# Performance work log

Hardware: AMD Instinct MI355X
Metric: run time of the kernel (lower is better)

The kernel has to match this reference:

```python
import jax, jax.numpy as jnp
import numpy as np

N_NODES = 1_000_000
N_EDGES = 32_000_000


def setup_inputs() -> dict:
    key = jax.random.key(0)
    k1, k2, k3, k4, k5 = jax.random.split(key, 5)
    state = jax.random.normal(k1, (N_NODES, 1), dtype=jnp.float32)
    edge_src = jax.random.randint(k2, (N_EDGES,), 0, N_NODES, dtype=jnp.int64)
    edge_dst = jax.random.randint(k3, (N_EDGES,), 0, N_NODES, dtype=jnp.int64)
    W = jax.random.normal(k4, (1, 2), dtype=jnp.float32)
    b = jax.random.normal(k5, (1,), dtype=jnp.float32)
    return {"state": state, "edge_src": edge_src, "edge_dst": edge_dst, "W": W, "b": b}


def reference(state, edge_src, edge_dst, W, b):
    # neighbor_sum[dst] += state[src]  (irregular gather + scatter-add)
    n = state.shape[0]
    messages = state[edge_src, 0]                              # [E]
    neighbor_sum = jax.ops.segment_sum(messages, edge_dst, num_segments=n)  # [n]
    x = jnp.concatenate([state, neighbor_sum[:, None]], axis=1)  # [n, 2]
    return x @ W.T + b                                           # [n, 1]
```

## Files before the change

kernel.cpp:

```cpp
#include <hip/hip_runtime.h>
#include <hip/hip_fp16.h>


#define NB_SHIFT 14
#define RANGE    (1 << NB_SHIFT)
#define NBALL    64
#define TPB      512
#define IPT      8
#define TILE     (TPB * IPT)
#define NWAVES   (TPB / 64)
#define NREP     4
#define GSPL     2
#define BPB      (NREP * GSPL)

typedef int   iv4 __attribute__((ext_vector_type(4)));
typedef float fv4 __attribute__((ext_vector_type(4)));
typedef unsigned uv4 __attribute__((ext_vector_type(4)));
typedef unsigned uv2 __attribute__((ext_vector_type(2)));

__device__ __forceinline__ void lds_fadd(float* p, float v) {
    unsigned addr = (unsigned)(uintptr_t)p;
    asm volatile("ds_add_f32 %0, %1" :: "v"(addr), "v"(v) : "memory");
}

__device__ __forceinline__ void lds_drain() {
    asm volatile("s_waitcnt lgkmcnt(0)" ::: "memory");
    __builtin_amdgcn_sched_barrier(0);
}

__global__ void k_init_cursors(int* __restrict__ cursors) {
    cursors[threadIdx.x] = 0;
}

__global__ __launch_bounds__(256) void k_cvt(const float* __restrict__ state,
                                             unsigned short* __restrict__ sh, int n4) {
    int i = blockIdx.x * blockDim.x + threadIdx.x;
    if (i >= n4) return;
    fv4 v = *(const fv4*)(state + i * 4);
    ushort4 h;
    h.x = __half_as_ushort(__float2half_rn(v[0]));
    h.y = __half_as_ushort(__float2half_rn(v[1]));
    h.z = __half_as_ushort(__float2half_rn(v[2]));
    h.w = __half_as_ushort(__float2half_rn(v[3]));
    *(ushort4*)(sh + i * 4) = h;
}

__global__ __launch_bounds__(TPB) void k_partition(
    const unsigned short* __restrict__ sh,
    const int* __restrict__ src,
    const int* __restrict__ dst,
    unsigned* __restrict__ records,
    int* __restrict__ cursors,
    int n_edges, int capR)
{
    __shared__ unsigned stage[TILE];
    __shared__ int cnt[NBALL];
    __shared__ int sbase[NBALL];
    __shared__ int gbase[NBALL];

    const int tid = threadIdx.x;
    const int rep = blockIdx.x & (NREP - 1);
    if (tid < NBALL) cnt[tid] = 0;

    const long long e0 = (long long)blockIdx.x * TILE + (long long)tid * IPT;

    unsigned rec[IPT];
    int bk[IPT];
    int pos[IPT];

    if (e0 + IPT <= (long long)n_edges) {
        const long long i4 = e0 >> 2;
        iv4 sA = __builtin_nontemporal_load((const iv4*)src + i4);
        iv4 sB = __builtin_nontemporal_load((const iv4*)src + i4 + 1);
        iv4 dA = __builtin_nontemporal_load((const iv4*)dst + i4);
        iv4 dB = __builtin_nontemporal_load((const iv4*)dst + i4 + 1);
        int s[IPT] = { sA[0], sA[1], sA[2], sA[3], sB[0], sB[1], sB[2], sB[3] };
        int d[IPT] = { dA[0], dA[1], dA[2], dA[3], dB[0], dB[1], dB[2], dB[3] };
        unsigned v[IPT];
        #pragma unroll
        for (int k = 0; k < IPT; ++k) v[k] = sh[s[k]];
        #pragma unroll
        for (int k = 0; k < IPT; ++k) {
            bk[k]  = d[k] >> NB_SHIFT;
            rec[k] = (v[k] << NB_SHIFT) | (unsigned)(d[k] & (RANGE - 1));
        }
    } else {
        #pragma unroll
        for (int k = 0; k < IPT; ++k) {
            long long e = e0 + k;
            if (e < n_edges) {
                int d = dst[e];
                unsigned v = sh[src[e]];
                bk[k]  = d >> NB_SHIFT;
                rec[k] = (v << NB_SHIFT) | (unsigned)(d & (RANGE - 1));
            } else {
                bk[k] = -1; rec[k] = 0;
            }
        }
    }
    __syncthreads();

    #pragma unroll
    for (int k = 0; k < IPT; ++k)
        if (bk[k] >= 0) pos[k] = atomicAdd(&cnt[bk[k]], 1);
    __syncthreads();

    if (tid < NBALL) {
        int h = cnt[tid];
        int v = h;
        #pragma unroll
        for (int off = 1; off < 64; off <<= 1) {
            int u = __shfl_up(v, off);
            if (tid >= off) v += u;
        }
        sbase[tid] = v - h;
        int he = (h + 1) & ~1;
        gbase[tid] = atomicAdd(&cursors[(tid << 2) | rep], he);
    }
    __syncthreads();

    #pragma unroll
    for (int k = 0; k < IPT; ++k)
        if (bk[k] >= 0) stage[sbase[bk[k]] + pos[k]] = rec[k];
    __syncthreads();

    const int wid = tid >> 6, lane = tid & 63;
    for (int b = wid; b < NBALL; b += NWAVES) {
        const int sb = sbase[b], h = cnt[b], gb = gbase[b];
        const int hp = (h + 1) >> 1;
        unsigned* dstp = records + (size_t)((b << 2) | rep) * capR + gb;
        for (int j = lane; j < hp; j += 64) {
            uv2 r;
            r[0] = stage[sb + 2 * j];
            r[1] = (2 * j + 1 < h) ? stage[sb + 2 * j + 1] : 0u;
            *(uv2*)(dstp + 2 * j) = r;
        }
    }
}

__global__ __launch_bounds__(1024) void k_bins(
    const unsigned* __restrict__ records,
    const int* __restrict__ cursors,
    float* __restrict__ partial,
    int capR)
{
    __shared__ float bins[RANGE];
    const int b   = blockIdx.x / BPB;
    const int sub = blockIdx.x % BPB;
    const int rep = sub >> 1;
    const int g   = sub & 1;
    const int cnt = cursors[(b << 2) | rep];
    const size_t base = (size_t)((b << 2) | rep) * capR;
    const int lo = (int)((long long)cnt * g       / GSPL) & ~1;
    const int hi = (g == GSPL - 1) ? cnt : ((int)((long long)cnt * (g + 1) / GSPL) & ~1);
    const int tid = threadIdx.x;

    fv4* bins4 = (fv4*)bins;
    for (int i = tid; i < RANGE / 4; i += 1024) bins4[i] = (fv4){0.f, 0.f, 0.f, 0.f};
    __syncthreads();

    int A = (lo + 3) & ~3; if (A > hi) A = hi;
    if (tid < A - lo) {
        unsigned r = records[base + lo + tid];
        float v = __half2float(__ushort_as_half((unsigned short)(r >> NB_SHIFT)));
        lds_fadd(&bins[r & (RANGE - 1)], v);
    }
    for (int i = A + tid * 4; i + 4 <= hi; i += 1024 * 4) {
        uv4 r = *(const uv4*)(records + base + i);
        #pragma unroll
        for (int k = 0; k < 4; ++k) {
            float v = __half2float(__ushort_as_half((unsigned short)(r[k] >> NB_SHIFT)));
            lds_fadd(&bins[r[k] & (RANGE - 1)], v);
        }
    }
    {
        int start = A + ((hi - A) & ~3);
        if (tid < hi - start) {
            unsigned r = records[base + start + tid];
            float v = __half2float(__ushort_as_half((unsigned short)(r >> NB_SHIFT)));
            lds_fadd(&bins[r & (RANGE - 1)], v);
        }
    }
    lds_drain();
    __syncthreads();

    float* p = partial + (size_t)blockIdx.x * RANGE;
    for (int i = tid; i < RANGE / 4; i += 1024)
        *((fv4*)p + i) = bins4[i];
}

__global__ __launch_bounds__(256) void k_finalize(
    const float* __restrict__ state,
    const float* __restrict__ partial,
    const float* __restrict__ W,
    const float* __restrict__ bias,
    float* __restrict__ out, int n)
{
    const int i = (blockIdx.x * blockDim.x + threadIdx.x) * 4;
    if (i >= n) return;
    const int b   = i >> NB_SHIFT;
    const int loc = i & (RANGE - 1);
    const float* pb = partial + (size_t)b * BPB * RANGE + loc;
    fv4 s = {0.f, 0.f, 0.f, 0.f};
    #pragma unroll
    for (int g = 0; g < BPB; ++g)
        s += *(const fv4*)(pb + (size_t)g * RANGE);
    const float w0 = W[0], w1 = W[1], bb = bias[0];
    fv4 st = *(const fv4*)(state + i);
    fv4 o;
    #pragma unroll
    for (int k = 0; k < 4; ++k) o[k] = fmaf(st[k], w0, fmaf(s[k], w1, bb));
    *(fv4*)(out + i) = o;
}

__global__ __launch_bounds__(256) void gnn_zero(float4* __restrict__ ws, int n4) {
    int i = blockIdx.x * blockDim.x + threadIdx.x;
    int stride = gridDim.x * blockDim.x;
    const float4 z = make_float4(0.f, 0.f, 0.f, 0.f);
    for (; i < n4; i += stride) ws[i] = z;
}

__global__ __launch_bounds__(256) void gnn_scatter_dev(const float* __restrict__ state,
                                                       const int* __restrict__ src,
                                                       const int* __restrict__ dst,
                                                       float* __restrict__ nsum,
                                                       int n_edges) {
    const int tid = blockIdx.x * blockDim.x + threadIdx.x;
    const int stride = gridDim.x * blockDim.x;
    const int n4 = n_edges >> 2;
    const int4* __restrict__ src4 = (const int4*)src;
    const int4* __restrict__ dst4 = (const int4*)dst;
    for (int i = tid; i < n4; i += stride) {
        int4 s = src4[i];
        int4 d = dst4[i];
        atomicAdd(&nsum[d.x], state[s.x]);
        atomicAdd(&nsum[d.y], state[s.y]);
        atomicAdd(&nsum[d.z], state[s.z]);
        atomicAdd(&nsum[d.w], state[s.w]);
    }
    for (int i = (n4 << 2) + tid; i < n_edges; i += stride)
        atomicAdd(&nsum[dst[i]], state[src[i]]);
}

__global__ __launch_bounds__(256) void gnn_finalize_flat(const float* __restrict__ state,
                                                         const float* __restrict__ nsum,
                                                         const float* __restrict__ W,
                                                         const float* __restrict__ b,
                                                         float* __restrict__ out, int n) {
    int i = blockIdx.x * blockDim.x + threadIdx.x;
    if (i < n) out[i] = fmaf(state[i], W[0], fmaf(nsum[i], W[1], b[0]));
}

extern "C" void kernel_launch(void* const* d_in, const int* in_sizes, int n_in,
                              void* d_out, int out_size, void* d_ws, size_t ws_size,
                              hipStream_t stream) {
    const float* state = (const float*)d_in[0];
    const int*   esrc  = (const int*)d_in[1];
    const int*   edst  = (const int*)d_in[2];
    const float* W     = (const float*)d_in[3];
    const float* b     = (const float*)d_in[4];
    float* out = (float*)d_out;

    const int n_nodes = in_sizes[0];
    const int n_edges = in_sizes[1];

    const int nbused = (n_nodes + RANGE - 1) >> NB_SHIFT;
    const long long lamR = (long long)n_edges * RANGE / n_nodes / NREP;
    int capR = (int)(lamR + lamR / 8 + 8192);
    capR = (capR + 3) & ~3;

    const size_t shOff   = 0;
    const size_t shBytes = ((size_t)n_nodes * 2 + 255) & ~(size_t)255;
    const size_t recOff  = shBytes;
    const size_t recBytes= ((size_t)NBALL * NREP * capR * 4 + 255) & ~(size_t)255;
    const size_t curOff  = recOff + recBytes;
    const size_t curBytes= (256 * sizeof(int) + 255) & ~(size_t)255;
    const size_t parOff  = curOff + curBytes;
    const size_t parBytes= (size_t)nbused * BPB * RANGE * sizeof(float);
    const size_t need    = parOff + parBytes;

    if (ws_size >= need && (n_nodes & 3) == 0 && (n_edges & 3) == 0) {
        unsigned short* sh = (unsigned short*)((char*)d_ws + shOff);
        unsigned* records  = (unsigned*)((char*)d_ws + recOff);
        int*      cursors  = (int*)((char*)d_ws + curOff);
        float*    partial  = (float*)((char*)d_ws + parOff);

        k_init_cursors<<<1, 256, 0, stream>>>(cursors);
        k_cvt<<<(n_nodes / 4 + 255) / 256, 256, 0, stream>>>(state, sh, n_nodes / 4);

        int tiles = (n_edges + TILE - 1) / TILE;
        k_partition<<<tiles, TPB, 0, stream>>>(sh, esrc, edst,
                                               records, cursors, n_edges, capR);

        k_bins<<<nbused * BPB, 1024, 0, stream>>>(records, cursors, partial, capR);

        int blocks = (n_nodes / 4 + 255) / 256;
        k_finalize<<<blocks, 256, 0, stream>>>(state, partial, W, b, out, n_nodes);
    } else {
        float* nsum = (float*)d_ws;
        int n4n = n_nodes >> 2;
        int zb = (n4n + 255) / 256; if (zb > 2048) zb = 2048;
        gnn_zero<<<zb, 256, 0, stream>>>((float4*)nsum, n4n);
        int work = n_edges >> 2;
        int sb = (work + 255) / 256; if (sb > 8192) sb = 8192;
        gnn_scatter_dev<<<sb, 256, 0, stream>>>(state, esrc, edst, nsum, n_edges);
        int fb = (n_nodes + 255) / 256;
        gnn_finalize_flat<<<fb, 256, 0, stream>>>(state, nsum, W, b, out, n_nodes);
    }
}
```

Measured before the change: 380.7 us.

## Split partition launch into three, prefetch records in bins loop, relax asm clobber

Result: slower. 408.5 us (+7.3%).

```diff
diff --git a/kernel.cpp b/kernel.cpp
--- a/kernel.cpp
+++ b/kernel.cpp
@@ -20,7 +20,7 @@
 
 __device__ __forceinline__ void lds_fadd(float* p, float v) {
     unsigned addr = (unsigned)(uintptr_t)p;
-    asm volatile("ds_add_f32 %0, %1" :: "v"(addr), "v"(v) : "memory");
+    asm volatile("ds_add_f32 %0, %1" :: "v"(addr), "v"(v));
 }
 
 __device__ __forceinline__ void lds_drain() {
@@ -51,7 +51,7 @@
     const int* __restrict__ dst,
     unsigned* __restrict__ records,
     int* __restrict__ cursors,
-    int n_edges, int capR)
+    int n_edges, int capR, int tile0)
 {
     __shared__ unsigned stage[TILE];
     __shared__ int cnt[NBALL];
@@ -59,10 +59,11 @@
     __shared__ int gbase[NBALL];
 
     const int tid = threadIdx.x;
-    const int rep = blockIdx.x & (NREP - 1);
+    const int bt  = blockIdx.x + tile0;
+    const int rep = bt & (NREP - 1);
     if (tid < NBALL) cnt[tid] = 0;
 
-    const long long e0 = (long long)blockIdx.x * TILE + (long long)tid * IPT;
+    const long long e0 = (long long)bt * TILE + (long long)tid * IPT;
 
     unsigned rec[IPT];
     int bk[IPT];
@@ -135,6 +136,14 @@
             r[1] = (2 * j + 1 < h) ? stage[sb + 2 * j + 1] : 0u;
             *(uv2*)(dstp + 2 * j) = r;
         }
+    }
+}
+
+__device__ __forceinline__ void add4(float* bins, uv4 r) {
+    #pragma unroll
+    for (int k = 0; k < 4; ++k) {
+        float v = __half2float(__ushort_as_half((unsigned short)(r[k] >> NB_SHIFT)));
+        lds_fadd(&bins[r[k] & (RANGE - 1)], v);
     }
 }
 
@@ -165,12 +174,19 @@
         float v = __half2float(__ushort_as_half((unsigned short)(r >> NB_SHIFT)));
         lds_fadd(&bins[r & (RANGE - 1)], v);
     }
-    for (int i = A + tid * 4; i + 4 <= hi; i += 1024 * 4) {
-        uv4 r = *(const uv4*)(records + base + i);
-        #pragma unroll
-        for (int k = 0; k < 4; ++k) {
-            float v = __half2float(__ushort_as_half((unsigned short)(r[k] >> NB_SHIFT)));
-            lds_fadd(&bins[r[k] & (RANGE - 1)], v);
+    {
+        const int stride = 1024 * 4;
+        int i = A + tid * 4;
+        if (i + 4 <= hi) {
+            uv4 r = *(const uv4*)(records + base + i);
+            int inext = i + stride;
+            while (inext + 4 <= hi) {
+                uv4 rn = *(const uv4*)(records + base + inext);
+                add4(bins, r);
+                r = rn;
+                inext += stride;
+            }
+            add4(bins, r);
         }
     }
     {
@@ -289,8 +305,13 @@
         k_cvt<<<(n_nodes / 4 + 255) / 256, 256, 0, stream>>>(state, sh, n_nodes / 4);
 
         int tiles = (n_edges + TILE - 1) / TILE;
-        k_partition<<<tiles, TPB, 0, stream>>>(sh, esrc, edst,
-                                               records, cursors, n_edges, capR);
+        int t1 = tiles / 3, t2 = tiles / 3, t3 = tiles - t1 - t2;
+        k_partition<<<t1, TPB, 0, stream>>>(sh, esrc, edst,
+                                            records, cursors, n_edges, capR, 0);
+        k_partition<<<t2, TPB, 0, stream>>>(sh, esrc, edst,
+                                            records, cursors, n_edges, capR, t1);
+        k_partition<<<t3, TPB, 0, stream>>>(sh, esrc, edst,
+                                            records, cursors, n_edges, capR, t1 + t2);
 
         k_bins<<<nbused * BPB, 1024, 0, stream>>>(records, cursors, partial, capR);
 
```
